# Optimization experiments

Measured on AMD Instinct MI355X. Metric: run time of the kernel, lower is better.

Reference implementation:

```python
import jax, jax.numpy as jnp
import numpy as np

NUM_SEQS = 16
NUM_HEADS = 32
NUM_KV_HEADS = 8
HEAD_SIZE = 128
BLOCK_SIZE = 16
X = 8  # vectorized key-cache packing factor
MAX_CTX = 4096
MAX_BLOCKS = MAX_CTX // BLOCK_SIZE
NUM_BLOCKS = NUM_SEQS * MAX_BLOCKS
SCALE = 0.08838834764831845  # 1/sqrt(128)
NEG_INF = -1e30


def setup_inputs() -> dict:
    key0 = jax.random.key(0)
    ks = jax.random.split(key0, 5)
    query = jax.random.normal(ks[0], (NUM_SEQS, 1, NUM_HEADS * HEAD_SIZE), jnp.float32)
    key = jax.random.normal(ks[1], (NUM_SEQS, 1, NUM_KV_HEADS * HEAD_SIZE), jnp.float32)
    value = jax.random.normal(ks[2], (NUM_SEQS, 1, NUM_KV_HEADS * HEAD_SIZE), jnp.float32)
    key_cache = jax.random.normal(ks[3], (NUM_BLOCKS, NUM_KV_HEADS, HEAD_SIZE // X, BLOCK_SIZE, X), jnp.float32)
    value_cache = jax.random.normal(ks[4], (NUM_BLOCKS, NUM_KV_HEADS, HEAD_SIZE, BLOCK_SIZE), jnp.float32)
    rng = np.random.default_rng(0)
    block_tables = rng.permutation(NUM_BLOCKS).reshape(NUM_SEQS, MAX_BLOCKS).astype(np.int32)
    context_lens = rng.integers(256, MAX_CTX + 1, size=(NUM_SEQS,)).astype(np.int32)
    last = context_lens - 1
    slots = block_tables[np.arange(NUM_SEQS), last // BLOCK_SIZE].astype(np.int64) * BLOCK_SIZE + (last % BLOCK_SIZE)
    slot_mapping = slots.reshape(NUM_SEQS, 1)
    return {
        'query': query, 'key': key, 'value': value,
        'key_cache': key_cache, 'value_cache': value_cache,
        'block_tables': jnp.asarray(block_tables),
        'context_lens': jnp.asarray(context_lens),
        'slot_mapping': jnp.asarray(slot_mapping),
    }


def _paged_attention_decode(query, key, value, key_cache, value_cache, block_tables, context_lens, slot_mapping):
    S, L1, hidden = query.shape  # L1 == 1 (decode)
    nb, kvH, _, bs, x = key_cache.shape
    D = value_cache.shape[2]
    H = hidden // D
    G = H // kvH  # queries per kv head
    maxB = block_tables.shape[1]

    q = query.reshape(S, H, D)
    k_new = key.reshape(S, kvH, D)
    v_new = value.reshape(S, kvH, D)

    # --- reshape_and_cache: write new K/V into paged caches ---
    sm = slot_mapping.reshape(-1)
    blk, off = sm // bs, sm % bs
    key_cache = key_cache.at[blk, :, :, off, :].set(k_new.reshape(S, kvH, D // x, x))
    value_cache = value_cache.at[blk, :, :, off].set(v_new)

    # --- gather paged KV via block tables ---
    # key_cache [nb,kvH,D/x,bs,x] -> [nb,kvH,bs,D]
    kc = key_cache.transpose(0, 1, 3, 2, 4).reshape(nb, kvH, bs, D)
    vc = value_cache.transpose(0, 1, 3, 2)  # [nb,kvH,bs,D]
    keys = kc[block_tables].transpose(0, 1, 3, 2, 4).reshape(S, maxB * bs, kvH, D)
    vals = vc[block_tables].transpose(0, 1, 3, 2, 4).reshape(S, maxB * bs, kvH, D)

    # --- GQA attention with context-length masking ---
    qg = q.reshape(S, kvH, G, D)
    scores = jnp.einsum('skgd,slkd->skgl', qg, keys) * jnp.asarray(SCALE, q.dtype)
    valid = jnp.arange(maxB * bs)[None, :] < context_lens[:, None]  # [S,L]
    scores = jnp.where(valid[:, None, None, :], scores, NEG_INF)
    probs = jax.nn.softmax(scores, axis=-1)
    out = jnp.einsum('skgl,slkd->skgd', probs, vals)
    return out.reshape(S, 1, H * D)


def reference(query, key, value, key_cache, value_cache, block_tables, context_lens, slot_mapping):
    return _paged_attention_decode(query, key, value, key_cache, value_cache,
                                   block_tables, context_lens, slot_mapping)
```

## Files before the change

kernel.cpp:

```cpp
#include <hip/hip_runtime.h>

#define NSEQ   16
#define KVH    8
#define NG     4
#define HD     128
#define BS     16
#define MAXB   256
#define PART   256
#define NPART  16
#define NITEMS (NSEQ * KVH * NPART)
#define WPT    64
#define PSTRIDE 520
#define REC_BYTES ((size_t)NITEMS * PSTRIDE * 4)
#define SCALE_F 0.08838834764831845f
#define NWORKERS 1024

typedef float vf4 __attribute__((ext_vector_type(4)));
__device__ __forceinline__ float4 ldnt4f(const float* p) {
    vf4 v = __builtin_nontemporal_load((const vf4*)p);
    return make_float4(v[0], v[1], v[2], v[3]);
}

__global__ __launch_bounds__(256) void pa_partial_kernel(
    const float* __restrict__ query,
    const float* __restrict__ key,
    const float* __restrict__ value,
    const float* __restrict__ key_cache,
    const float* __restrict__ value_cache,
    const int*   __restrict__ block_tables,
    const int*   __restrict__ context_lens,
    float*       __restrict__ ws,
    unsigned int* __restrict__ counter)
{
    __shared__ float p_lds[4][NG][WPT];
    __shared__ float o_lds[4][NG * HD];
    __shared__ float ml_lds[4][8];
    __shared__ int   item_s;

    const int tid  = threadIdx.x;
    const int wv   = tid >> 6;
    const int lane = tid & 63;

    for (;;) {
        if (tid == 0) item_s = (int)atomicAdd(counter, 1u);
        __syncthreads();
        const int item = item_s;
        __syncthreads();
        if (item >= NITEMS) return;

        const int p   = item & (NPART - 1);
        const int kvh = (item >> 4) & (KVH - 1);
        const int s   = item >> 7;
        const int ctx = context_lens[s];
        const int t0  = p * PART;
        if (t0 >= ctx) continue;

        const bool ntp = ((p & 3) == 3);

        const int tw0  = t0 + wv * WPT;
        const bool wact = (tw0 < ctx);

        const float* q = query + ((size_t)s * KVH + kvh) * (NG * HD);

        float m_w = -1e30f;
        float l_w[NG] = {0.f, 0.f, 0.f, 0.f};

        if (wact) {
            const int t  = tw0 + lane;
            const int bt = block_tables[s * MAXB + (t >> 4)];
            const float* kb = key_cache + (size_t)bt * (KVH * HD * BS)
                                        + (size_t)kvh * (HD * BS) + (t & 15) * 8;

            float sc[NG] = {0.f, 0.f, 0.f, 0.f};
            if (ntp) {
                #pragma unroll
                for (int j = 0; j < 16; ++j) {
                    const float4 ka = ldnt4f(kb + j * 128);
                    const float4 kc = ldnt4f(kb + j * 128 + 4);
                    #pragma unroll
                    for (int g = 0; g < NG; ++g) {
                        sc[g] += q[g * HD + j * 8 + 0] * ka.x + q[g * HD + j * 8 + 1] * ka.y
                               + q[g * HD + j * 8 + 2] * ka.z + q[g * HD + j * 8 + 3] * ka.w
                               + q[g * HD + j * 8 + 4] * kc.x + q[g * HD + j * 8 + 5] * kc.y
                               + q[g * HD + j * 8 + 6] * kc.z + q[g * HD + j * 8 + 7] * kc.w;
                    }
                }
            } else {
                #pragma unroll
                for (int j = 0; j < 16; ++j) {
                    const float4 ka = *(const float4*)(kb + j * 128);
                    const float4 kc = *(const float4*)(kb + j * 128 + 4);
                    #pragma unroll
                    for (int g = 0; g < NG; ++g) {
                        sc[g] += q[g * HD + j * 8 + 0] * ka.x + q[g * HD + j * 8 + 1] * ka.y
                               + q[g * HD + j * 8 + 2] * ka.z + q[g * HD + j * 8 + 3] * ka.w
                               + q[g * HD + j * 8 + 4] * kc.x + q[g * HD + j * 8 + 5] * kc.y
                               + q[g * HD + j * 8 + 6] * kc.z + q[g * HD + j * 8 + 7] * kc.w;
                    }
                }
            }

            if (t == ctx - 1) {
                const float4* kn4 = (const float4*)(key + ((size_t)s * KVH + kvh) * HD);
                float ns[NG] = {0.f, 0.f, 0.f, 0.f};
                #pragma unroll
                for (int c = 0; c < 32; ++c) {
                    const float4 k4 = kn4[c];
                    #pragma unroll
                    for (int g = 0; g < NG; ++g) {
                        ns[g] += q[g * HD + c * 4 + 0] * k4.x + q[g * HD + c * 4 + 1] * k4.y
                               + q[g * HD + c * 4 + 2] * k4.z + q[g * HD + c * 4 + 3] * k4.w;
                    }
                }
                #pragma unroll
                for (int g = 0; g < NG; ++g) sc[g] = ns[g];
            }

            float mv;
            if (t < ctx) {
                #pragma unroll
                for (int g = 0; g < NG; ++g) sc[g] *= SCALE_F;
                mv = fmaxf(fmaxf(sc[0], sc[1]), fmaxf(sc[2], sc[3]));
            } else {
                #pragma unroll
                for (int g = 0; g < NG; ++g) sc[g] = -1e30f;
                mv = -1e30f;
            }

            #pragma unroll
            for (int o = 32; o; o >>= 1) mv = fmaxf(mv, __shfl_xor(mv, o));
            m_w = mv;

            float pr[NG];
            #pragma unroll
            for (int g = 0; g < NG; ++g) {
                pr[g] = __expf(sc[g] - m_w);
                p_lds[wv][g][lane] = pr[g];
                l_w[g] = pr[g];
            }
            #pragma unroll
            for (int o = 32; o; o >>= 1) {
                l_w[0] += __shfl_xor(l_w[0], o);
                l_w[1] += __shfl_xor(l_w[1], o);
                l_w[2] += __shfl_xor(l_w[2], o);
                l_w[3] += __shfl_xor(l_w[3], o);
            }
        }

        if (lane == 0) {
            ml_lds[wv][0] = m_w;
            #pragma unroll
            for (int g = 0; g < NG; ++g) ml_lds[wv][1 + g] = l_w[g];
        }

        if (wact) {
            int btv[4];
            #pragma unroll
            for (int b = 0; b < 4; ++b)
                btv[b] = block_tables[s * MAXB + (tw0 >> 4) + b];

            const int tl = ctx - 1 - tw0;
            const int tq = lane & 3;
            const int dl = lane >> 2;

            float acc[NG][8];
            #pragma unroll
            for (int g = 0; g < NG; ++g)
                #pragma unroll
                for (int sub = 0; sub < 8; ++sub) acc[g][sub] = 0.f;

            #pragma unroll
            for (int b = 0; b < 4; ++b) {
                if (tw0 + b * 16 < ctx) {
                    const float* vb = value_cache + (size_t)btv[b] * (KVH * HD * BS)
                                                  + (size_t)kvh * (HD * BS);
                    float4 p4[NG];
                    #pragma unroll
                    for (int g = 0; g < NG; ++g)
                        p4[g] = *(const float4*)&p_lds[wv][g][b * 16 + tq * 4];
                    if (ntp) {
                        #pragma unroll
                        for (int sub = 0; sub < 8; ++sub) {
                            const float4 v4 = ldnt4f(vb + sub * 256 + lane * 4);
                            #pragma unroll
                            for (int g = 0; g < NG; ++g)
                                acc[g][sub] += p4[g].x * v4.x + p4[g].y * v4.y
                                             + p4[g].z * v4.z + p4[g].w * v4.w;
                        }
                    } else {
                        #pragma unroll
                        for (int sub = 0; sub < 8; ++sub) {
                            const float4 v4 = *(const float4*)(vb + sub * 256 + lane * 4);
                            #pragma unroll
                            for (int g = 0; g < NG; ++g)
                                acc[g][sub] += p4[g].x * v4.x + p4[g].y * v4.y
                                             + p4[g].z * v4.z + p4[g].w * v4.w;
                        }
                    }
                }
            }

            #pragma unroll
            for (int g = 0; g < NG; ++g)
                #pragma unroll
                for (int sub = 0; sub < 8; ++sub) {
                    float a = acc[g][sub];
                    a += __shfl_xor(a, 1);
                    a += __shfl_xor(a, 2);
                    acc[g][sub] = a;
                }

            if (tl >= 0 && tl < WPT) {
                const int btn = block_tables[s * MAXB + ((ctx - 1) >> 4)];
                const float* vbn = value_cache + (size_t)btn * (KVH * HD * BS)
                                               + (size_t)kvh * (HD * BS) + ((ctx - 1) & 15);
                const float* vrow = value + ((size_t)s * KVH + kvh) * HD;
                #pragma unroll
                for (int sub = 0; sub < 8; ++sub) {
                    const int d = sub * 16 + dl;
                    const float dv = vrow[d] - vbn[d * BS];
                    #pragma unroll
                    for (int g = 0; g < NG; ++g)
                        acc[g][sub] += p_lds[wv][g][tl] * dv;
                }
            }

            if (tq == 0) {
                #pragma unroll
                for (int g = 0; g < NG; ++g)
                    #pragma unroll
                    for (int sub = 0; sub < 8; ++sub)
                        o_lds[wv][g * HD + sub * 16 + dl] = acc[g][sub];
            }
        } else {
            #pragma unroll
            for (int i = 0; i < 8; ++i) o_lds[wv][i * 64 + lane] = 0.f;
        }

        __syncthreads();

        const float m0 = ml_lds[0][0], m1 = ml_lds[1][0], m2 = ml_lds[2][0], m3 = ml_lds[3][0];
        const float M  = fmaxf(fmaxf(m0, m1), fmaxf(m2, m3));
        const float w0 = __expf(m0 - M), w1 = __expf(m1 - M);
        const float w2 = __expf(m2 - M), w3 = __expf(m3 - M);

        float* rec = ws + (size_t)item * PSTRIDE;
        #pragma unroll
        for (int r = 0; r < 2; ++r) {
            const int idx = tid + r * 256;
            rec[idx] = w0 * o_lds[0][idx] + w1 * o_lds[1][idx]
                     + w2 * o_lds[2][idx] + w3 * o_lds[3][idx];
        }
        if (tid < NG) {
            rec[512 + tid] = w0 * ml_lds[0][1 + tid] + w1 * ml_lds[1][1 + tid]
                           + w2 * ml_lds[2][1 + tid] + w3 * ml_lds[3][1 + tid];
        }
        if (tid == 4) rec[516] = M;
    }
}

__global__ __launch_bounds__(128) void pa_reduce_kernel(
    const float* __restrict__ ws,
    const int*   __restrict__ context_lens,
    float*       __restrict__ out)
{
    const int b    = blockIdx.x;
    const int g    = b & 3;
    const int pair = b >> 2;
    const int s    = pair >> 3;
    const int kvh  = pair & 7;
    const int ctx  = context_lens[s];
    const int np   = (ctx + PART - 1) / PART;

    const int d = threadIdx.x;
    const float* base = ws + (size_t)pair * NPART * PSTRIDE;

    float M = -1e30f;
    for (int p2 = 0; p2 < np; ++p2) M = fmaxf(M, base[p2 * PSTRIDE + 516]);

    float L = 0.f, acc = 0.f;
    for (int p2 = 0; p2 < np; ++p2) {
        const float* rec = base + p2 * PSTRIDE;
        const float w = __expf(rec[516] - M);
        L   += w * rec[512 + g];
        acc += w * rec[g * HD + d];
    }

    out[(size_t)s * (KVH * NG * HD) + (size_t)(kvh * NG + g) * HD + d] = acc / L;
}

extern "C" void kernel_launch(void* const* d_in, const int* in_sizes, int n_in,
                              void* d_out, int out_size, void* d_ws, size_t ws_size,
                              hipStream_t stream) {
    const float* query       = (const float*)d_in[0];
    const float* key         = (const float*)d_in[1];
    const float* value       = (const float*)d_in[2];
    const float* key_cache   = (const float*)d_in[3];
    const float* value_cache = (const float*)d_in[4];
    const int*   block_tables  = (const int*)d_in[5];
    const int*   context_lens  = (const int*)d_in[6];

    float* out = (float*)d_out;
    float* ws  = (float*)d_ws;
    unsigned int* counter = (unsigned int*)((char*)d_ws + REC_BYTES);

    (void)hipMemsetAsync(counter, 0, sizeof(unsigned int), stream);
    pa_partial_kernel<<<NWORKERS, 256, 0, stream>>>(
        query, key, value, key_cache, value_cache, block_tables, context_lens, ws, counter);
    pa_reduce_kernel<<<NSEQ * KVH * NG, 128, 0, stream>>>(ws, context_lens, out);
}
```

Before: 82.49 us.

## Fuse partial and reduce kernels via grid-wide completion counter

Merges the split-K reduction into the partial-attention kernel: each worker block bumps a second counter once it runs out of items, and the first 128 blocks spin until every worker has finished, then combine the partition records for one (seq, kv-head) pair using coherent atomic loads. This removes one kernel launch and its launch gap. In exchange it relies on all 1024 blocks being co-resident; if they are not, the spinning blocks can deadlock. Reduction parallelism also drops from 512 blocks of 128 threads to 128 blocks of 256 threads, and the blocks do nothing while they wait for the slowest worker.

```diff
diff --git a/kernel.cpp b/kernel.cpp
--- a/kernel.cpp
+++ b/kernel.cpp
@@ -9,6 +9,7 @@
 #define PART   256
 #define NPART  16
 #define NITEMS (NSEQ * KVH * NPART)
+#define NPAIRS (NSEQ * KVH)
 #define WPT    64
 #define PSTRIDE 520
 #define REC_BYTES ((size_t)NITEMS * PSTRIDE * 4)
@@ -21,7 +22,11 @@
     return make_float4(v[0], v[1], v[2], v[3]);
 }
 
-__global__ __launch_bounds__(256) void pa_partial_kernel(
+__device__ __forceinline__ float cohld(const float* p) {
+    return __hip_atomic_load(p, __ATOMIC_RELAXED, __HIP_MEMORY_SCOPE_AGENT);
+}
+
+__global__ __launch_bounds__(256) void pa_fused_kernel(
     const float* __restrict__ query,
     const float* __restrict__ key,
     const float* __restrict__ value,
@@ -30,7 +35,8 @@
     const int*   __restrict__ block_tables,
     const int*   __restrict__ context_lens,
     float*       __restrict__ ws,
-    unsigned int* __restrict__ counter)
+    unsigned int* __restrict__ counter,
+    float*       __restrict__ out)
 {
     __shared__ float p_lds[4][NG][WPT];
     __shared__ float o_lds[4][NG * HD];
@@ -42,11 +48,11 @@
     const int lane = tid & 63;
 
     for (;;) {
-        if (tid == 0) item_s = (int)atomicAdd(counter, 1u);
+        if (tid == 0) item_s = (int)atomicAdd(&counter[0], 1u);
         __syncthreads();
         const int item = item_s;
         __syncthreads();
-        if (item >= NITEMS) return;
+        if (item >= NITEMS) break;
 
         const int p   = item & (NPART - 1);
         const int kvh = (item >> 4) & (KVH - 1);
@@ -257,36 +263,47 @@
         }
         if (tid == 4) rec[516] = M;
     }
-}
-
-__global__ __launch_bounds__(128) void pa_reduce_kernel(
-    const float* __restrict__ ws,
-    const int*   __restrict__ context_lens,
-    float*       __restrict__ out)
-{
-    const int b    = blockIdx.x;
-    const int g    = b & 3;
-    const int pair = b >> 2;
-    const int s    = pair >> 3;
-    const int kvh  = pair & 7;
-    const int ctx  = context_lens[s];
-    const int np   = (ctx + PART - 1) / PART;
-
-    const int d = threadIdx.x;
-    const float* base = ws + (size_t)pair * NPART * PSTRIDE;
-
-    float M = -1e30f;
-    for (int p2 = 0; p2 < np; ++p2) M = fmaxf(M, base[p2 * PSTRIDE + 516]);
-
-    float L = 0.f, acc = 0.f;
-    for (int p2 = 0; p2 < np; ++p2) {
-        const float* rec = base + p2 * PSTRIDE;
-        const float w = __expf(rec[516] - M);
-        L   += w * rec[512 + g];
-        acc += w * rec[g * HD + d];
+
+    __syncthreads();
+    if (tid == 0) {
+        __threadfence();
+        atomicAdd(&counter[1], 1u);
     }
 
-    out[(size_t)s * (KVH * NG * HD) + (size_t)(kvh * NG + g) * HD + d] = acc / L;
+    if (blockIdx.x < NPAIRS) {
+        if (tid == 0) {
+            while (__hip_atomic_load(&counter[1], __ATOMIC_ACQUIRE,
+                                     __HIP_MEMORY_SCOPE_AGENT) < NWORKERS)
+                __builtin_amdgcn_s_sleep(2);
+        }
+        __syncthreads();
+        __threadfence();
+
+        const int pair = blockIdx.x;
+        const int s    = pair >> 3;
+        const int kvh  = pair & 7;
+        const int ctx  = context_lens[s];
+        const int np   = (ctx + PART - 1) / PART;
+        const float* base = ws + (size_t)pair * NPART * PSTRIDE;
+
+        float M = -1e30f;
+        for (int p2 = 0; p2 < np; ++p2)
+            M = fmaxf(M, cohld(base + p2 * PSTRIDE + 516));
+
+        #pragma unroll
+        for (int half = 0; half < 2; ++half) {
+            const int g = (tid >> 7) + half * 2;
+            const int d = tid & 127;
+            float L = 0.f, acc = 0.f;
+            for (int p2 = 0; p2 < np; ++p2) {
+                const float* rec = base + p2 * PSTRIDE;
+                const float w = __expf(cohld(rec + 516) - M);
+                L   += w * cohld(rec + 512 + g);
+                acc += w * cohld(rec + g * HD + d);
+            }
+            out[(size_t)s * (KVH * NG * HD) + (size_t)(kvh * NG + g) * HD + d] = acc / L;
+        }
+    }
 }
 
 extern "C" void kernel_launch(void* const* d_in, const int* in_sizes, int n_in,
@@ -304,8 +321,8 @@
     float* ws  = (float*)d_ws;
     unsigned int* counter = (unsigned int*)((char*)d_ws + REC_BYTES);
 
-    (void)hipMemsetAsync(counter, 0, sizeof(unsigned int), stream);
-    pa_partial_kernel<<<NWORKERS, 256, 0, stream>>>(
-        query, key, value, key_cache, value_cache, block_tables, context_lens, ws, counter);
-    pa_reduce_kernel<<<NSEQ * KVH * NG, 128, 0, stream>>>(ws, context_lens, out);
+    (void)hipMemsetAsync(counter, 0, 2 * sizeof(unsigned int), stream);
+    pa_fused_kernel<<<NWORKERS, 256, 0, stream>>>(
+        query, key, value, key_cache, value_cache, block_tables, context_lens,
+        ws, counter, out);
 }
```

Measured after the change: 192.5 us. +133.4%, slower.
